# Kernel tuning notes

Measured on AMD Instinct MI355X. Metric: run time of the kernel, lower is better.

The kernel has to match this reference:

```python
import jax, jax.numpy as jnp
import numpy as np

B, N, DIM = 4, 2048, 768
HEADS, DH, DEPTH = 12, 64, 4
W = 35                     # hard-coded window size
P = DIM // 2               # window-embedding proj dim
V4 = DIM // 4              # window-embedding value dim
PB = DIM // 4              # dynamic pos-bias MLP width
FF = DIM * 4
NEG = float(np.finfo(np.float32).max)


def setup_inputs() -> dict:
    key = jax.random.key(0)
    ks = iter(jax.random.split(key, 32))
    r = lambda shape: jax.random.normal(next(ks), shape, jnp.float32) * 0.02
    return dict(
        x=jax.random.normal(next(ks), (B, N, DIM), jnp.float32),
        mask=jnp.zeros((B, N), bool),
        ln1_g=jnp.ones((DEPTH, DIM)), ln1_b=jnp.zeros((DEPTH, DIM)),
        qkv_W=r((DEPTH, DIM, 3 * HEADS * DH)),
        temp=jnp.full((DEPTH,), 15.5, jnp.float32),
        we_lin_W=r((DEPTH, DIM, P)), we_q_W=r((DEPTH, P, P)),
        we_k_W=r((DEPTH, DIM, P)), we_v_W=r((DEPTH, DIM, V4)),
        we_bos=jnp.zeros((DEPTH, V4)), we_scale=jnp.ones((DEPTH,)),
        out_W=r((DEPTH, DIM + V4, DIM)),
        ln2_g=jnp.ones((DEPTH, DIM)), ln2_b=jnp.zeros((DEPTH, DIM)),
        glu_W=r((DEPTH, DIM, 2 * FF)), glu_b=jnp.zeros((DEPTH, 2 * FF)),
        ffo_W=r((DEPTH, FF, DIM)), ffo_b=jnp.zeros((DEPTH, DIM)),
        pb_W1=r((1, PB)), pb_b1=jnp.zeros((PB,)),
        pb_W2=r((PB, PB)), pb_b2=jnp.zeros((PB,)),
        pb_W3=r((PB, HEADS)), pb_b3=jnp.zeros((HEADS,)),
    )


def _ln(x, g, b):
    m = x.mean(-1, keepdims=True)
    v = ((x - m) ** 2).mean(-1, keepdims=True)
    return (x - m) * jax.lax.rsqrt(v + 1e-5) * g + b


def _l2norm(t):
    # matches F.normalize(p=2, dim=-1): x / max(||x||, 1e-12)
    return t / jnp.maximum(jnp.linalg.norm(t, axis=-1, keepdims=True), 1e-12)


def _pos_bias(n, W1, b1, W2, b2, W3, b3):
    # DynamicPositionBias(dim=PB, depth=2): Linear->ReLU, Linear->ReLU, Linear
    pos = jnp.arange(-n + 1, n, dtype=jnp.float32)[:, None]          # (2n-1, 1)
    h = jax.nn.relu(pos @ W1 + b1)
    h = jax.nn.relu(h @ W2 + b2)
    out = h @ W3 + b3                                                # (2n-1, H)
    idx = jnp.arange(n)[:, None] - jnp.arange(n)[None, :] + n - 1    # (n, n)
    return jnp.transpose(out[idx], (2, 0, 1))                        # (H, n, n)


def _sinu(n, scale):
    # ScaledSinuEmbedding over proj dim P
    inv = 1.0 / (10000.0 ** (jnp.arange(0, P, 2, dtype=jnp.float32) / P))
    s = jnp.arange(n, dtype=jnp.float32)[:, None] * inv[None, :]
    return jnp.concatenate([jnp.sin(s), jnp.cos(s)], -1) * scale     # (n, P)


def _forward(x, mask, ln1_g, ln1_b, qkv_W, temp, we_lin_W, we_q_W, we_k_W,
             we_v_W, we_bos, we_scale, out_W, ln2_g, ln2_b, glu_W, glu_b,
             ffo_W, ffo_b, pb_W1, pb_b1, pb_W2, pb_b2, pb_W3, pb_b3):
    Bz, Nn, _ = x.shape
    pad = (-Nn) % W
    nw = (Nn + pad) // W
    bias = _pos_bias(W, pb_W1, pb_b1, pb_W2, pb_b2, pb_W3, pb_b3)    # (H, W, W)
    causal = jnp.triu(jnp.ones((W, W), bool), 1)
    mpad = jnp.concatenate([mask, jnp.ones((Bz, pad), bool)], 1).reshape(Bz, nw, W)
    valid = ~mpad                                                    # (B, w, n)
    amask = ~(valid[:, None, :, :, None] & valid[:, None, :, None, :]) | causal
    we_mask = mpad[:, :, None, :]                                    # (B, w, 1, n)
    lengths = jnp.maximum(valid.sum(-1), 1).astype(jnp.float32)[..., None, None]
    sinu35 = _sinu(W, 1.0)                                           # (W, P)

    for l in range(DEPTH):
        # ---- PreNorm + windowed cosine attention ----
        h = _ln(x, ln1_g[l], ln1_b[l])
        hp = jnp.concatenate([h, jnp.zeros((Bz, pad, DIM), h.dtype)], 1)
        hp = hp.reshape(Bz, nw, W, DIM)
        qkv = (hp @ qkv_W[l]).reshape(Bz, nw, W, HEADS, DH, 3)
        q, k, v = (jnp.transpose(qkv[..., i], (0, 3, 1, 2, 4)) for i in range(3))
        q, k = _l2norm(q), _l2norm(k)
        dots = jnp.einsum('bhwid,bhwjd->bhwij', q, k) * temp[l] + bias[None, :, None]
        dots = jnp.where(amask, -NEG, dots)
        attn = jax.nn.softmax(dots, axis=-1)
        o = jnp.einsum('bhwij,bhwjd->bhwid', attn, v)
        o = jnp.transpose(o, (0, 2, 3, 1, 4)).reshape(Bz, nw, W, HEADS * DH)
        # ---- window_embeddings: pooled prev-window embedding attention ----
        we = jnp.where(mpad[..., None], 0.0, o) @ we_lin_W[l]         # (B,w,n,P)
        we = jax.nn.relu(we.sum(-2, keepdims=True) / lengths)        # (B,w,1,P)
        wq = we @ we_q_W[l]
        k2 = o @ we_k_W[l] + sinu35 * we_scale[l]
        v2 = o @ we_v_W[l]
        d2 = jnp.einsum('bwid,bwjd->bwij', wq, k2) * (P ** -0.5)
        d2 = jnp.where(we_mask, -NEG, d2)
        o2 = jnp.einsum('bwij,bwjd->bwid', jax.nn.softmax(d2, -1), v2)  # (B,w,1,V4)
        bos = jnp.broadcast_to(we_bos[l], (Bz, 1, 1, V4))
        o2 = jnp.concatenate([bos, o2], 1)[:, :-1]                   # shift by one window
        o = jnp.concatenate([o, jnp.broadcast_to(o2, (Bz, nw, W, V4))], -1)
        o = (o @ out_W[l]).reshape(Bz, nw * W, DIM)[:, :Nn]
        x = x + o
        # ---- PreNorm + GLU feed-forward ----
        h2 = _ln(x, ln2_g[l], ln2_b[l])
        a, g = jnp.split(h2 @ glu_W[l] + glu_b[l], 2, axis=-1)
        x = x + ((a * jax.nn.silu(g)) @ ffo_W[l] + ffo_b[l])
    return x


def reference(x, mask, ln1_g, ln1_b, qkv_W, temp, we_lin_W, we_q_W, we_k_W,
              we_v_W, we_bos, we_scale, out_W, ln2_g, ln2_b, glu_W, glu_b,
              ffo_W, ffo_b, pb_W1, pb_b1, pb_W2, pb_b2, pb_W3, pb_b3):
    return _forward(x, mask, ln1_g, ln1_b, qkv_W, temp, we_lin_W, we_q_W,
                    we_k_W, we_v_W, we_bos, we_scale, out_W, ln2_g, ln2_b,
                    glu_W, glu_b, ffo_W, ffo_b, pb_W1, pb_b1, pb_W2, pb_b2,
                    pb_W3, pb_b3)
```

## Files before the change

kernel.cpp:

```cpp
#include <hip/hip_runtime.h>
#include <hip/hip_bf16.h>
#include <cstddef>
#include <cstdint>

#define B_ 4
#define N_ 2048
#define DIM_ 768
#define HEADS_ 12
#define DH_ 64
#define DEPTH_ 4
#define W_ 35
#define P_ 384
#define V4_ 192
#define FF_ 3072
#define NW_ 59
#define NPB_ (NW_*W_)
#define NTOK_ (B_*N_)
#define NWB_ (B_*NW_)
#define NTP_ (NWB_*W_)
#define NTPA_ 8448
#define NEG_ 3.402823466e+38f

typedef __bf16 bf16x8 __attribute__((ext_vector_type(8)));
typedef float  f32x4  __attribute__((ext_vector_type(4)));

#define GLOAD16(g, l) __builtin_amdgcn_global_load_lds( \
    (const __attribute__((address_space(1))) uint32_t*)(g), \
    (__attribute__((address_space(3))) uint32_t*)(l), 16, 0, 0)


__global__ __launch_bounds__(192) void posbias1_k(
    const float* __restrict__ W1, const float* __restrict__ b1,
    const float* __restrict__ W2, const float* __restrict__ b2,
    const float* __restrict__ W3, const float* __restrict__ b3,
    float* __restrict__ outk)
{
    __shared__ float h1[192];
    __shared__ float h2[192];
    int i = blockIdx.x;
    int tid = threadIdx.x;
    float pos = (float)(i - 34);
    h1[tid] = fmaxf(pos*W1[tid] + b1[tid], 0.f);
    __syncthreads();
    float s = b2[tid];
    for (int k=0;k<192;k++) s += h1[k]*W2[k*192+tid];
    h2[tid] = fmaxf(s, 0.f);
    __syncthreads();
    if (tid < 12){
        float o = b3[tid];
        for (int k=0;k<192;k++) o += h2[k]*W3[k*12+tid];
        outk[i*12+tid] = o;
    }
}

__global__ void posbias2_k(const float* __restrict__ outk, float* __restrict__ bias)
{
    int e = threadIdx.x + blockIdx.x*blockDim.x;
    if (e >= HEADS_*W_*W_) return;
    int h=e/(W_*W_); int rem=e%(W_*W_); int i=rem/W_; int j=rem%W_;
    bias[e] = outk[(i-j+W_-1)*12 + h];
}

__global__ void sinu_k(float* __restrict__ sinu)
{
    int i = blockIdx.x;
    int k = threadIdx.x;
    float inv = powf(10000.f, -(float)k/192.f);
    float s = (float)i * inv;
    sinu[i*P_ + k]       = sinf(s);
    sinu[i*P_ + 192 + k] = cosf(s);
}

__global__ void len_k(const unsigned char* __restrict__ mask, float* __restrict__ len)
{
    int bw = threadIdx.x + blockIdx.x*blockDim.x;
    if (bw >= NWB_) return;
    int b = bw / NW_, w = bw % NW_;
    int cnt = 0;
    for (int t=0;t<W_;t++){
        int g = w*W_ + t;
        if (g < N_ && mask[b*N_+g]==0) cnt++;
    }
    len[bw] = fmaxf((float)cnt, 1.f);
}

__global__ __launch_bounds__(256) void pack_k(
    const float* __restrict__ W, __bf16* __restrict__ Bp,
    int N, int Ncov, int Nld, size_t lsW, size_t lsB, int qkvperm, int ncol0)
{
    int n = blockIdx.x*256 + threadIdx.x;
    int k8 = blockIdx.y, l = blockIdx.z;
    if (n >= Ncov) return;
    bf16x8 v;
    if (n < N){
        int sn = n;
        if (qkvperm){ int s = n/768, hd = n - s*768; sn = hd*3 + s; }
        const float* w = W + lsW*l + (size_t)k8*8*N + sn;
        #pragma unroll
        for (int e=0;e<8;e++) v[e] = (__bf16)w[(size_t)e*N];
    } else {
        #pragma unroll
        for (int e=0;e<8;e++) v[e] = (__bf16)0.f;
    }
    *(bf16x8*)(Bp + lsB*l + ((size_t)k8*Nld + ncol0 + n)*8) = v;
}

__global__ __launch_bounds__(256) void ln_k(
    const float* __restrict__ x, const float* __restrict__ g,
    const float* __restrict__ b, __bf16* __restrict__ out,
    const float* __restrict__ o2p, int padded)
{
    int r = blockIdx.x;
    int tid = threadIdx.x;
    int lane = tid & 63, wave = tid >> 6;
    int row = r; bool real = true;
    if (padded){
        int bb = r / NPB_, n = r % NPB_;
        if (n >= N_) real = false;
        row = bb*N_ + n;
    }
    float v0=0,v1=0,v2=0;
    if (real){
        const float* xr = x + (size_t)row*DIM_;
        v0 = xr[tid]; v1 = xr[tid+256]; v2 = xr[tid+512];
        if (o2p){
            int bb = row / N_, nn = row % N_;
            const float* op = o2p + (size_t)(bb*NW_ + nn/W_)*DIM_;
            v0 += op[tid]; v1 += op[tid+256]; v2 += op[tid+512];
        }
    }
    float s1 = v0+v1+v2;
    float s2 = v0*v0+v1*v1+v2*v2;
    #pragma unroll
    for (int off=32; off; off>>=1){
        s1 += __shfl_xor(s1, off);
        s2 += __shfl_xor(s2, off);
    }
    __shared__ float a1[4], a2[4];
    if (lane==0){ a1[wave]=s1; a2[wave]=s2; }
    __syncthreads();
    s1 = a1[0]+a1[1]+a1[2]+a1[3];
    s2 = a2[0]+a2[1]+a2[2]+a2[3];
    float m   = s1 * (1.f/768.f);
    float var = s2 * (1.f/768.f) - m*m;
    float inv = rsqrtf(var + 1e-5f);
    __bf16* o = out + (size_t)r*DIM_;
    if (!real){ o[tid]=(__bf16)0.f; o[tid+256]=(__bf16)0.f; o[tid+512]=(__bf16)0.f; return; }
    o[tid]     = (__bf16)((v0-m)*inv*g[tid]     + b[tid]);
    o[tid+256] = (__bf16)((v1-m)*inv*g[tid+256] + b[tid+256]);
    o[tid+512] = (__bf16)((v2-m)*inv*g[tid+512] + b[tid+512]);
}

template<int EPI, bool DUAL, int BM, int NT>
__global__ __launch_bounds__(NT) void mgemm_k(
    const __bf16* __restrict__ A, const __bf16* __restrict__ Bp,
    float* __restrict__ Cf, __bf16* __restrict__ Cb, float* __restrict__ Cf2,
    float* __restrict__ Cx,
    const float* __restrict__ bias, const float* __restrict__ extra,
    const float* __restrict__ scale_ptr,
    int M, int K, int Nc, int Nld, int Cld)
{
    constexpr int BN = DUAL ? 64 : 128;
    constexpr int WM = NT / 128;
    constexpr int RS = BM / WM;
    constexpr int MF = RS / 16;
    constexpr int NF = (BN/2) / 16;
    constexpr int AS = BM * 32;
    constexpr int BS = BN * 32;
    __shared__ alignas(16) __bf16 As[3*AS];
    __shared__ alignas(16) __bf16 Bs[3*BS];
    __shared__ alignas(16) __bf16 Gs[DUAL ? 3*BS : 16];
    const int tid = threadIdx.x;
    const int lane = tid & 63, wave = tid >> 6;
    const int wr = wave >> 1, wc = wave & 1;
    const int m0 = blockIdx.y*BM;
    const int n0 = blockIdx.x*BN;
    const int lk = lane >> 4, lr = lane & 15;
    f32x4 acc[MF][NF] = {};
    f32x4 acc2[DUAL?MF:1][NF] = {};

    auto stage = [&](int wb, int kt){
        const int k0 = kt * 32;
        #pragma unroll
        for (int q = 0; q < (BM*4)/NT; q++){
            int i = tid + q*NT;
            int r = i & (BM-1), k8 = i / BM;
            GLOAD16(A + (size_t)(m0 + r)*K + k0 + k8*8, As + (size_t)(wb*AS + i*8));
        }
        if constexpr (!DUAL){
            #pragma unroll
            for (int q = 0; q < 512/NT; q++){
                int i = tid + q*NT;
                int n = i & 127, k8 = i >> 7;
                GLOAD16(Bp + ((size_t)(k0/8 + k8)*Nld + n0 + n)*8, Bs + (size_t)(wb*BS + i*8));
            }
        } else if constexpr (NT == 512){
            int i = tid & 255;
            int n = i & 63, k8 = i >> 6;
            size_t goff = ((size_t)(k0/8 + k8)*Nld + n0 + n + (tid < 256 ? 0 : FF_))*8;
            __bf16* dst = (tid < 256 ? Bs : Gs) + (size_t)(wb*BS + i*8);
            GLOAD16(Bp + goff, dst);
        } else {
            const int n = tid & 63, k8 = tid >> 6;
            GLOAD16(Bp + ((size_t)(k0/8 + k8)*Nld + n0 + n)*8,       Bs + (size_t)(wb*BS + tid*8));
            GLOAD16(Bp + ((size_t)(k0/8 + k8)*Nld + n0 + n + FF_)*8, Gs + (size_t)(wb*BS + tid*8));
        }
    };

    const int nk = K >> 5;
    stage(0, 0);
    if (nk > 1) stage(1, 1);
    int rb = 0;
    for (int t = 0; t < nk; ++t){
        if (t == nk-1) asm volatile("s_waitcnt vmcnt(0)" ::: "memory");
        else           asm volatile("s_waitcnt vmcnt(3)" ::: "memory");
        __builtin_amdgcn_s_barrier();
        __builtin_amdgcn_sched_barrier(0);
        if (t + 2 < nk){
            int wb = rb + 2; if (wb >= 3) wb -= 3;
            stage(wb, t+2);
        }
        const __bf16* as = As + (size_t)rb*AS;
        bf16x8 af[MF];
        #pragma unroll
        for (int m=0;m<MF;m++)
            af[m] = *(const bf16x8*)(as + ((size_t)(lk*BM + wr*RS + m*16 + lr))*8);
        const __bf16* bs = Bs + (size_t)rb*BS;
        bf16x8 bfr[NF];
        #pragma unroll
        for (int n=0;n<NF;n++)
            bfr[n] = *(const bf16x8*)(bs + ((size_t)(lk*BN + wc*(BN/2) + n*16 + lr))*8);
        #pragma unroll
        for (int m=0;m<MF;m++)
            #pragma unroll
            for (int n=0;n<NF;n++)
                acc[m][n] = __builtin_amdgcn_mfma_f32_16x16x32_bf16(af[m], bfr[n], acc[m][n], 0,0,0);
        if constexpr (DUAL){
            const __bf16* gs = Gs + (size_t)rb*BS;
            bf16x8 gfr[NF];
            #pragma unroll
            for (int n=0;n<NF;n++)
                gfr[n] = *(const bf16x8*)(gs + ((size_t)(lk*BN + wc*(BN/2) + n*16 + lr))*8);
            #pragma unroll
            for (int m=0;m<MF;m++)
                #pragma unroll
                for (int n=0;n<NF;n++)
                    acc2[m][n] = __builtin_amdgcn_mfma_f32_16x16x32_bf16(af[m], gfr[n], acc2[m][n], 0,0,0);
        }
        rb++; if (rb >= 3) rb = 0;
    }

    const int lq = lane >> 4;
    #pragma unroll
    for (int m=0;m<MF;m++){
        #pragma unroll
        for (int r=0;r<4;r++){
            int row = m0 + wr*RS + m*16 + lq*4 + r;
            if (row >= M) continue;
            #pragma unroll
            for (int n=0;n<NF;n++){
                int col = n0 + wc*(BN/2) + n*16 + lr;
                if (col >= Nc) continue;
                float v = acc[m][n][r];
                if (EPI==1){
                    Cb[(size_t)row*Cld + col] = (__bf16)v;
                } else if (EPI==3){
                    int bb = row / N_, nn = row % N_;
                    int bw = bb*NW_ + nn/W_;
                    Cf[(size_t)row*Cld + col] += v + bias[col]
                        + extra[(size_t)bw*DIM_ + col];
                } else if (EPI==4){
                    float a_ = v + bias[col];
                    float g_ = acc2[m][n][r] + bias[col + FF_];
                    Cb[(size_t)row*Cld + col] = (__bf16)(a_ * (g_ / (1.f + expf(-g_))));
                } else if (EPI==8){
                    if (col < P_){
                        int tt = (row % NPB_) % W_;
                        Cf[(size_t)row*P_ + col] = v + extra[tt*P_ + col]*scale_ptr[0];
                    } else if (col < 576){
                        Cf2[(size_t)row*V4_ + (col - P_)] = v;
                    } else {
                        int bb = row / NPB_, nn = row % NPB_;
                        if (nn < N_)
                            Cx[(size_t)(bb*N_ + nn)*DIM_ + (col - 576)] += v;
                    }
                }
            }
        }
    }
}

__global__ __launch_bounds__(256) void gemm0_k(
    const float* __restrict__ A, const float* __restrict__ Bw,
    float* __restrict__ C, int M, int K, int Nc, int ldb)
{
    __shared__ float As[16][65];
    __shared__ float Bs[16][65];
    const int m0 = blockIdx.y*64, n0 = blockIdx.x*64;
    const int tid = threadIdx.x;
    const int ty = tid>>4, tx = tid&15;
    float acc[4][4] = {};
    for (int k0=0; k0<K; k0+=16){
        #pragma unroll
        for (int i=0;i<4;i++){
            int e = tid + i*256;
            int m = e>>4, kk = e&15;
            int mg = m0+m;
            As[kk][m] = (mg < M) ? A[(size_t)mg*K + k0+kk] : 0.f;
        }
        #pragma unroll
        for (int i=0;i<4;i++){
            int e = tid + i*256;
            int kk = e>>6, n = e&63;
            Bs[kk][n] = Bw[(size_t)(k0+kk)*ldb + n0+n];
        }
        __syncthreads();
        #pragma unroll
        for (int kk=0;kk<16;kk++){
            float a[4], bv[4];
            #pragma unroll
            for (int i=0;i<4;i++) a[i] = As[kk][ty*4+i];
            #pragma unroll
            for (int j=0;j<4;j++) bv[j] = Bs[kk][tx*4+j];
            #pragma unroll
            for (int i=0;i<4;i++)
                #pragma unroll
                for (int j=0;j<4;j++) acc[i][j] += a[i]*bv[j];
        }
        __syncthreads();
    }
    #pragma unroll
    for (int i=0;i<4;i++){
        int mg = m0 + ty*4 + i;
        if (mg >= M) continue;
        #pragma unroll
        for (int j=0;j<4;j++){
            int c = n0 + tx*4 + j;
            if (c >= Nc) continue;
            C[(size_t)mg*Nc + c] = acc[i][j];
        }
    }
}

__global__ __launch_bounds__(256) void attn_k(
    const __bf16* __restrict__ qkv, const unsigned char* __restrict__ mask,
    const float* __restrict__ bias, const float* __restrict__ temp_p,
    __bf16* __restrict__ obuf, float* __restrict__ osum)
{
    int bid = blockIdx.x;
    int w = bid % NW_;
    int h = (bid / NW_) % HEADS_;
    int b = bid / (NW_*HEADS_);
    int tid = threadIdx.x;
    __shared__ float qs[W_*DH_], ks[W_*DH_], vs[W_*DH_];
    __shared__ float sc[W_*W_];
    __shared__ float osacc[4][64];
    __shared__ int vf[W_];
    int bw = b*NW_ + w;
    int rbase = bw*W_;
    for (int e=tid; e<W_*DH_; e+=256){
        int t=e>>6, d=e&63;
        size_t idx = (size_t)(rbase+t)*(3*DIM_) + h*DH_ + d;
        qs[e]=(float)qkv[idx];
        ks[e]=(float)qkv[idx+768];
        vs[e]=(float)qkv[idx+1536];
    }
    if (tid < W_){
        int g = w*W_ + tid;
        vf[tid] = (g < N_) && (mask[b*N_+g]==0);
    }
    __syncthreads();
    for (int e=tid; e<2*W_; e+=256){
        float* src = (e<W_)? qs : ks;
        int t = (e<W_)? e : e-W_;
        float s=0;
        for (int d=0;d<DH_;d++){ float v=src[t*DH_+d]; s+=v*v; }
        float inv = 1.f / fmaxf(sqrtf(s), 1e-12f);
        for (int d=0;d<DH_;d++) src[t*DH_+d] *= inv;
    }
    __syncthreads();
    float temp = temp_p[0];
    for (int e=tid; e<W_*W_; e+=256){
        int i=e/W_, j=e%W_;
        float s;
        if (!vf[i] || !vf[j] || j>i) s = -NEG_;
        else {
            float acc=0;
            for (int d=0;d<DH_;d++) acc += qs[i*DH_+d]*ks[j*DH_+d];
            s = acc*temp + bias[(h*W_+i)*W_+j];
        }
        sc[e]=s;
    }
    __syncthreads();
    if (tid < W_){
        int i=tid;
        float mx=-INFINITY;
        for (int j=0;j<W_;j++) mx=fmaxf(mx, sc[i*W_+j]);
        float sum=0;
        for (int j=0;j<W_;j++){ float e_=expf(sc[i*W_+j]-mx); sc[i*W_+j]=e_; sum+=e_; }
        float inv=1.f/sum;
        for (int j=0;j<W_;j++) sc[i*W_+j]*=inv;
    }
    __syncthreads();
    int wavei = tid >> 6, d = tid & 63;
    float psum = 0.f;
    for (int i = wavei; i < W_; i += 4){
        float s=0;
        for (int j=0;j<W_;j++) s += sc[i*W_+j]*vs[j*DH_+d];
        obuf[(size_t)(rbase+i)*DIM_ + h*DH_ + d] = (__bf16)s;
        if (vf[i]) psum += s;
    }
    osacc[wavei][d] = psum;
    __syncthreads();
    if (tid < 64)
        osum[(size_t)bw*DIM_ + h*DH_ + tid] =
            osacc[0][tid]+osacc[1][tid]+osacc[2][tid]+osacc[3][tid];
}

__global__ __launch_bounds__(384) void wefuse_k(
    const float* __restrict__ osum, const float* __restrict__ we_lin,
    const float* __restrict__ we_q, const float* __restrict__ k2,
    const float* __restrict__ v2, const unsigned char* __restrict__ mask,
    const float* __restrict__ len, float* __restrict__ o2)
{
    int bw = blockIdx.x;
    int b = bw / NW_, w = bw % NW_;
    int tid = threadIdx.x;
    __shared__ float osr[768], werr[384], wqr[384], pp[W_];
    osr[tid]     = osum[(size_t)bw*DIM_ + tid];
    osr[tid+384] = osum[(size_t)bw*DIM_ + tid + 384];
    __syncthreads();
    float invlen = 1.f / len[bw];
    float s = 0;
    for (int k=0;k<768;k++) s += osr[k]*we_lin[(size_t)k*P_ + tid];
    werr[tid] = fmaxf(s*invlen, 0.f);
    __syncthreads();
    s = 0;
    for (int k=0;k<384;k++) s += werr[k]*we_q[(size_t)k*P_ + tid];
    wqr[tid] = s;
    __syncthreads();
    if (tid < W_){
        int g = w*W_ + tid;
        bool val = (g < N_) && (mask[b*N_+g]==0);
        float sv = -NEG_;
        if (val){
            float acc=0;
            const float* kr = k2 + (size_t)(bw*W_+tid)*P_;
            for (int c=0;c<P_;c++) acc += wqr[c]*kr[c];
            sv = acc * 0.05103103630798287f;
        }
        pp[tid]=sv;
    }
    __syncthreads();
    if (tid==0){
        float mx=-INFINITY;
        for (int j=0;j<W_;j++) mx=fmaxf(mx,pp[j]);
        float sum=0;
        for (int j=0;j<W_;j++){ float e=expf(pp[j]-mx); pp[j]=e; sum+=e; }
        float inv=1.f/sum;
        for (int j=0;j<W_;j++) pp[j]*=inv;
    }
    __syncthreads();
    if (tid < V4_){
        float sv=0;
        for (int j=0;j<W_;j++) sv += pp[j]*v2[(size_t)(bw*W_+j)*V4_ + tid];
        o2[(size_t)bw*V4_ + tid] = sv;
    }
}

__global__ void o2shift_k(const float* __restrict__ o2, const float* __restrict__ bos,
                          float* __restrict__ o2u)
{
    int e = threadIdx.x + blockIdx.x*blockDim.x;
    if (e >= NWB_*V4_) return;
    int bw = e / V4_, c = e % V4_;
    int w = bw % NW_;
    o2u[e] = (w==0) ? bos[c] : o2[e - V4_];
}


extern "C" void kernel_launch(void* const* d_in, const int* in_sizes, int n_in,
                              void* d_out, int out_size, void* d_ws, size_t ws_size,
                              hipStream_t stream)
{
    const float* x       = (const float*)d_in[0];
    const unsigned char* mask = (const unsigned char*)d_in[1];
    const float* ln1_g   = (const float*)d_in[2];
    const float* ln1_b   = (const float*)d_in[3];
    const float* qkv_W   = (const float*)d_in[4];
    const float* temp    = (const float*)d_in[5];
    const float* we_lin_W= (const float*)d_in[6];
    const float* we_q_W  = (const float*)d_in[7];
    const float* we_k_W  = (const float*)d_in[8];
    const float* we_v_W  = (const float*)d_in[9];
    const float* we_bos  = (const float*)d_in[10];
    const float* we_scale= (const float*)d_in[11];
    const float* out_W   = (const float*)d_in[12];
    const float* ln2_g   = (const float*)d_in[13];
    const float* ln2_b   = (const float*)d_in[14];
    const float* glu_W   = (const float*)d_in[15];
    const float* glu_b   = (const float*)d_in[16];
    const float* ffo_W   = (const float*)d_in[17];
    const float* ffo_b   = (const float*)d_in[18];
    const float* pb_W1   = (const float*)d_in[19];
    const float* pb_b1   = (const float*)d_in[20];
    const float* pb_W2   = (const float*)d_in[21];
    const float* pb_b2   = (const float*)d_in[22];
    const float* pb_W3   = (const float*)d_in[23];
    const float* pb_b3   = (const float*)d_in[24];

    float* xc = (float*)d_out;

    char* p = (char*)d_ws;
    auto alloc = [&](size_t bytes)->char* {
        char* r = p; p += (bytes + 255) & ~(size_t)255; return r;
    };
    float* f_outk = (float*)alloc((size_t)69*12*4);
    float* f_bias = (float*)alloc((size_t)HEADS_*W_*W_*4);
    float* f_sinu = (float*)alloc((size_t)W_*P_*4);
    float* f_len  = (float*)alloc((size_t)NWB_*4);
    float* f_osum = (float*)alloc((size_t)NWB_*DIM_*4);
    float* f_o2   = (float*)alloc((size_t)NWB_*V4_*4);
    float* f_o2u  = (float*)alloc((size_t)NWB_*V4_*4);
    float* f_o2p  = (float*)alloc((size_t)NWB_*DIM_*4);
    __bf16* w_qkv = (__bf16*)alloc((size_t)DEPTH_*96*2304*8*2);
    __bf16* w_kvo = (__bf16*)alloc((size_t)DEPTH_*96*1408*8*2);
    __bf16* w_glu = (__bf16*)alloc((size_t)DEPTH_*96*6144*8*2);
    __bf16* w_ffo = (__bf16*)alloc((size_t)DEPTH_*384*768*8*2);
    char* arena = p;
    __bf16* f_hpad = (__bf16*)alloc((size_t)NTPA_*DIM_*2);
    __bf16* f_qkvb = (__bf16*)alloc((size_t)NTP_*3*DIM_*2);
    __bf16* f_obuf = (__bf16*)alloc((size_t)NTPA_*DIM_*2);
    float*  f_k2   = (float*)alloc((size_t)NTP_*P_*4);
    float*  f_v2   = (float*)alloc((size_t)NTP_*V4_*4);
    __bf16* f_h2 = (__bf16*)arena;
    __bf16* f_ag = (__bf16*)(arena + (((size_t)NTOK_*DIM_*2 + 255) & ~(size_t)255));
    (void)ws_size; (void)in_sizes; (void)n_in; (void)out_size;

    hipMemcpyAsync(xc, x, (size_t)NTOK_*DIM_*sizeof(float),
                   hipMemcpyDeviceToDevice, stream);
    posbias1_k<<<69,192,0,stream>>>(pb_W1,pb_b1,pb_W2,pb_b2,pb_W3,pb_b3,f_outk);
    posbias2_k<<<(HEADS_*W_*W_+255)/256,256,0,stream>>>(f_outk, f_bias);
    sinu_k<<<W_,192,0,stream>>>(f_sinu);
    len_k<<<1,256,0,stream>>>(mask, f_len);
    pack_k<<<dim3(9,96,DEPTH_),256,0,stream>>>(qkv_W, w_qkv, 2304, 2304, 2304,
        (size_t)768*2304, (size_t)96*2304*8, 1, 0);
    pack_k<<<dim3(2,96,DEPTH_),256,0,stream>>>(we_k_W, w_kvo, 384, 384, 1408,
        (size_t)768*384, (size_t)96*1408*8, 0, 0);
    pack_k<<<dim3(1,96,DEPTH_),256,0,stream>>>(we_v_W, w_kvo, 192, 192, 1408,
        (size_t)768*192, (size_t)96*1408*8, 0, 384);
    pack_k<<<dim3(4,96,DEPTH_),256,0,stream>>>(out_W, w_kvo, 768, 832, 1408,
        (size_t)960*768, (size_t)96*1408*8, 0, 576);
    pack_k<<<dim3(24,96,DEPTH_),256,0,stream>>>(glu_W, w_glu, 6144, 6144, 6144,
        (size_t)768*6144, (size_t)96*6144*8, 0, 0);
    pack_k<<<dim3(3,384,DEPTH_),256,0,stream>>>(ffo_W, w_ffo, 768, 768, 768,
        (size_t)3072*768, (size_t)384*768*8, 0, 0);

    for (int l=0;l<DEPTH_;l++){
        ln_k<<<NTP_,256,0,stream>>>(xc, ln1_g+l*DIM_, ln1_b+l*DIM_, f_hpad,
            nullptr, 1);
        mgemm_k<1,false,128,256><<<dim3(18,65),256,0,stream>>>(f_hpad,
            w_qkv + (size_t)l*96*2304*8, nullptr, f_qkvb, nullptr, nullptr,
            nullptr, nullptr, nullptr, NTP_, DIM_, 3*DIM_, 3*DIM_, 3*DIM_);
        attn_k<<<B_*HEADS_*NW_,256,0,stream>>>(f_qkvb, mask, f_bias, temp+l,
            f_obuf, f_osum);
        mgemm_k<8,false,64,256><<<dim3(11,130),256,0,stream>>>(f_obuf,
            w_kvo + (size_t)l*96*1408*8, f_k2, nullptr, f_v2, xc,
            nullptr, f_sinu, we_scale+l, NTP_, DIM_, 1344, 1408, 0);
        wefuse_k<<<NWB_,384,0,stream>>>(f_osum, we_lin_W + (size_t)l*DIM_*P_,
            we_q_W + (size_t)l*P_*P_, f_k2, f_v2, mask, f_len, f_o2);
        o2shift_k<<<(NWB_*V4_+255)/256,256,0,stream>>>(f_o2, we_bos+l*V4_, f_o2u);
        gemm0_k<<<dim3(12,4),256,0,stream>>>(f_o2u,
            out_W + (size_t)l*(DIM_+V4_)*DIM_ + (size_t)DIM_*DIM_,
            f_o2p, NWB_, V4_, DIM_, DIM_);

        ln_k<<<NTOK_,256,0,stream>>>(xc, ln2_g+l*DIM_, ln2_b+l*DIM_, f_h2,
            f_o2p, 0);
        mgemm_k<4,true,256,512><<<dim3(48,32),512,0,stream>>>(f_h2,
            w_glu + (size_t)l*96*6144*8, nullptr, f_ag, nullptr, nullptr,
            glu_b + (size_t)l*2*FF_, nullptr, nullptr,
            NTOK_, DIM_, FF_, 2*FF_, FF_);
        mgemm_k<3,false,64,256><<<dim3(6,128),256,0,stream>>>(f_ag,
            w_ffo + (size_t)l*384*768*8, xc, nullptr, nullptr, nullptr,
            ffo_b + (size_t)l*DIM_, f_o2p, nullptr,
            NTOK_, FF_, DIM_, DIM_, DIM_);
    }
}
```

Before: 2.283 ms.

## Precompute GEMM load pointers, add MFMA priority, and shrink GLU tile to 128x256

The GEMM kernel now computes its global load pointers once and advances them by a fixed step each k-tile, instead of recomputing 64-bit offsets per stage. It wraps the MFMA block in s_setprio so waves that are computing get scheduling priority. The GLU dual GEMM drops from a 256-row, 512-thread tile to a 128-row, 256-thread tile with twice as many blocks, which changes occupancy and data reuse. The wait count is adjusted to match the number of loads per stage. The smaller GLU tile cuts A-tile reuse per block and raises the total load traffic for B.

```diff
diff --git a/kernel.cpp b/kernel.cpp
--- a/kernel.cpp
+++ b/kernel.cpp
@@ -151,8 +151,8 @@
     o[tid+512] = (__bf16)((v2-m)*inv*g[tid+512] + b[tid+512]);
 }
 
-template<int EPI, bool DUAL, int BM, int NT>
-__global__ __launch_bounds__(NT) void mgemm_k(
+template<int EPI, bool DUAL, int BM>
+__global__ __launch_bounds__(256) void mgemm_k(
     const __bf16* __restrict__ A, const __bf16* __restrict__ Bp,
     float* __restrict__ Cf, __bf16* __restrict__ Cb, float* __restrict__ Cf2,
     float* __restrict__ Cx,
@@ -161,12 +161,13 @@
     int M, int K, int Nc, int Nld, int Cld)
 {
     constexpr int BN = DUAL ? 64 : 128;
-    constexpr int WM = NT / 128;
-    constexpr int RS = BM / WM;
+    constexpr int RS = BM / 2;
     constexpr int MF = RS / 16;
     constexpr int NF = (BN/2) / 16;
     constexpr int AS = BM * 32;
     constexpr int BS = BN * 32;
+    constexpr int ALD = BM / 64;
+    constexpr int NL  = ALD + 2;
     __shared__ alignas(16) __bf16 As[3*AS];
     __shared__ alignas(16) __bf16 Bs[3*BS];
     __shared__ alignas(16) __bf16 Gs[DUAL ? 3*BS : 16];
@@ -179,74 +180,89 @@
     f32x4 acc[MF][NF] = {};
     f32x4 acc2[DUAL?MF:1][NF] = {};
 
-    auto stage = [&](int wb, int kt){
-        const int k0 = kt * 32;
-        #pragma unroll
-        for (int q = 0; q < (BM*4)/NT; q++){
-            int i = tid + q*NT;
-            int r = i & (BM-1), k8 = i / BM;
-            GLOAD16(A + (size_t)(m0 + r)*K + k0 + k8*8, As + (size_t)(wb*AS + i*8));
-        }
+    const __bf16* aP[ALD];
+    int aO[ALD];
+    #pragma unroll
+    for (int q=0;q<ALD;q++){
+        int i = tid + q*256;
+        int r = i & (BM-1), k8 = i / BM;
+        aP[q] = A + (size_t)(m0+r)*K + k8*8;
+        aO[q] = i*8;
+    }
+    const __bf16* bP[2];
+    int bO[2];
+    if constexpr (!DUAL){
+        #pragma unroll
+        for (int q=0;q<2;q++){
+            int i = tid + q*256;
+            int n = i & 127, k8 = i >> 7;
+            bP[q] = Bp + ((size_t)k8*Nld + n0 + n)*8;
+            bO[q] = i*8;
+        }
+    } else {
+        int n = tid & 63, k8 = tid >> 6;
+        bP[0] = Bp + ((size_t)k8*Nld + n0 + n)*8;
+        bP[1] = bP[0] + (size_t)FF_*8;
+        bO[0] = tid*8;
+        bO[1] = tid*8;
+    }
+    const size_t bStep = (size_t)Nld*32;
+
+    auto stage = [&](int wb){
+        #pragma unroll
+        for (int q=0;q<ALD;q++)
+            GLOAD16(aP[q], As + wb*AS + aO[q]);
         if constexpr (!DUAL){
-            #pragma unroll
-            for (int q = 0; q < 512/NT; q++){
-                int i = tid + q*NT;
-                int n = i & 127, k8 = i >> 7;
-                GLOAD16(Bp + ((size_t)(k0/8 + k8)*Nld + n0 + n)*8, Bs + (size_t)(wb*BS + i*8));
-            }
-        } else if constexpr (NT == 512){
-            int i = tid & 255;
-            int n = i & 63, k8 = i >> 6;
-            size_t goff = ((size_t)(k0/8 + k8)*Nld + n0 + n + (tid < 256 ? 0 : FF_))*8;
-            __bf16* dst = (tid < 256 ? Bs : Gs) + (size_t)(wb*BS + i*8);
-            GLOAD16(Bp + goff, dst);
+            GLOAD16(bP[0], Bs + wb*BS + bO[0]);
+            GLOAD16(bP[1], Bs + wb*BS + bO[1]);
         } else {
-            const int n = tid & 63, k8 = tid >> 6;
-            GLOAD16(Bp + ((size_t)(k0/8 + k8)*Nld + n0 + n)*8,       Bs + (size_t)(wb*BS + tid*8));
-            GLOAD16(Bp + ((size_t)(k0/8 + k8)*Nld + n0 + n + FF_)*8, Gs + (size_t)(wb*BS + tid*8));
-        }
+            GLOAD16(bP[0], Bs + wb*BS + bO[0]);
+            GLOAD16(bP[1], Gs + wb*BS + bO[1]);
+        }
+        #pragma unroll
+        for (int q=0;q<ALD;q++) aP[q] += 32;
+        bP[0] += bStep; bP[1] += bStep;
     };
 
     const int nk = K >> 5;
-    stage(0, 0);
-    if (nk > 1) stage(1, 1);
+    stage(0);
+    stage(1);
     int rb = 0;
     for (int t = 0; t < nk; ++t){
-        if (t == nk-1) asm volatile("s_waitcnt vmcnt(0)" ::: "memory");
-        else           asm volatile("s_waitcnt vmcnt(3)" ::: "memory");
+        if (t == nk-1)              asm volatile("s_waitcnt vmcnt(0)" ::: "memory");
+        else if constexpr (NL == 3) asm volatile("s_waitcnt vmcnt(3)" ::: "memory");
+        else                        asm volatile("s_waitcnt vmcnt(4)" ::: "memory");
         __builtin_amdgcn_s_barrier();
         __builtin_amdgcn_sched_barrier(0);
         if (t + 2 < nk){
             int wb = rb + 2; if (wb >= 3) wb -= 3;
-            stage(wb, t+2);
-        }
-        const __bf16* as = As + (size_t)rb*AS;
-        bf16x8 af[MF];
-        #pragma unroll
-        for (int m=0;m<MF;m++)
-            af[m] = *(const bf16x8*)(as + ((size_t)(lk*BM + wr*RS + m*16 + lr))*8);
-        const __bf16* bs = Bs + (size_t)rb*BS;
-        bf16x8 bfr[NF];
-        #pragma unroll
-        for (int n=0;n<NF;n++)
-            bfr[n] = *(const bf16x8*)(bs + ((size_t)(lk*BN + wc*(BN/2) + n*16 + lr))*8);
+            stage(wb);
+        }
+        const __bf16* as = As + rb*AS + (size_t)(lk*BM + wr*RS + lr)*8;
+        const __bf16* bs = Bs + rb*BS + (size_t)(lk*BN + wc*(BN/2) + lr)*8;
+        bf16x8 af[MF], bfr[NF];
+        #pragma unroll
+        for (int m=0;m<MF;m++) af[m] = *(const bf16x8*)(as + m*128);
+        #pragma unroll
+        for (int n=0;n<NF;n++) bfr[n] = *(const bf16x8*)(bs + n*128);
+        __builtin_amdgcn_s_setprio(1);
         #pragma unroll
         for (int m=0;m<MF;m++)
             #pragma unroll
             for (int n=0;n<NF;n++)
                 acc[m][n] = __builtin_amdgcn_mfma_f32_16x16x32_bf16(af[m], bfr[n], acc[m][n], 0,0,0);
         if constexpr (DUAL){
-            const __bf16* gs = Gs + (size_t)rb*BS;
+            const __bf16* gs = Gs + rb*BS + (size_t)(lk*BN + wc*(BN/2) + lr)*8;
             bf16x8 gfr[NF];
             #pragma unroll
-            for (int n=0;n<NF;n++)
-                gfr[n] = *(const bf16x8*)(gs + ((size_t)(lk*BN + wc*(BN/2) + n*16 + lr))*8);
+            for (int n=0;n<NF;n++) gfr[n] = *(const bf16x8*)(gs + n*128);
             #pragma unroll
             for (int m=0;m<MF;m++)
                 #pragma unroll
                 for (int n=0;n<NF;n++)
                     acc2[m][n] = __builtin_amdgcn_mfma_f32_16x16x32_bf16(af[m], gfr[n], acc2[m][n], 0,0,0);
         }
+        __builtin_amdgcn_s_setprio(0);
         rb++; if (rb >= 3) rb = 0;
     }
 
@@ -559,12 +575,12 @@
     for (int l=0;l<DEPTH_;l++){
         ln_k<<<NTP_,256,0,stream>>>(xc, ln1_g+l*DIM_, ln1_b+l*DIM_, f_hpad,
             nullptr, 1);
-        mgemm_k<1,false,128,256><<<dim3(18,65),256,0,stream>>>(f_hpad,
+        mgemm_k<1,false,128><<<dim3(18,65),256,0,stream>>>(f_hpad,
             w_qkv + (size_t)l*96*2304*8, nullptr, f_qkvb, nullptr, nullptr,
             nullptr, nullptr, nullptr, NTP_, DIM_, 3*DIM_, 3*DIM_, 3*DIM_);
         attn_k<<<B_*HEADS_*NW_,256,0,stream>>>(f_qkvb, mask, f_bias, temp+l,
             f_obuf, f_osum);
-        mgemm_k<8,false,64,256><<<dim3(11,130),256,0,stream>>>(f_obuf,
+        mgemm_k<8,false,64><<<dim3(11,130),256,0,stream>>>(f_obuf,
             w_kvo + (size_t)l*96*1408*8, f_k2, nullptr, f_v2, xc,
             nullptr, f_sinu, we_scale+l, NTP_, DIM_, 1344, 1408, 0);
         wefuse_k<<<NWB_,384,0,stream>>>(f_osum, we_lin_W + (size_t)l*DIM_*P_,
@@ -576,11 +592,11 @@
 
         ln_k<<<NTOK_,256,0,stream>>>(xc, ln2_g+l*DIM_, ln2_b+l*DIM_, f_h2,
             f_o2p, 0);
-        mgemm_k<4,true,256,512><<<dim3(48,32),512,0,stream>>>(f_h2,
+        mgemm_k<4,true,128><<<dim3(48,64),256,0,stream>>>(f_h2,
             w_glu + (size_t)l*96*6144*8, nullptr, f_ag, nullptr, nullptr,
             glu_b + (size_t)l*2*FF_, nullptr, nullptr,
             NTOK_, DIM_, FF_, 2*FF_, FF_);
-        mgemm_k<3,false,64,256><<<dim3(6,128),256,0,stream>>>(f_ag,
+        mgemm_k<3,false,64><<<dim3(6,128),256,0,stream>>>(f_ag,
             w_ffo + (size_t)l*384*768*8, xc, nullptr, nullptr, nullptr,
             ffo_b + (size_t)l*DIM_, f_o2p, nullptr,
             NTOK_, FF_, DIM_, DIM_, DIM_);
```

Result: faster. 2.216 ms (-2.9%).
